# Performance work log

Measured on AMD Instinct MI355X. Metric: run time of the kernel, lower is better.

Reference implementation:

```python
import jax, jax.numpy as jnp
import numpy as np

KERNEL_SIZE = 5


def setup_inputs() -> dict:
    key = jax.random.key(0)
    k1, k2 = jax.random.split(key)
    x = jax.random.normal(k1, (4, 32, 256, 256), dtype=jnp.float32)
    kernel = jax.random.normal(k2, (4, KERNEL_SIZE * KERNEL_SIZE, 256, 256), dtype=jnp.float32)
    return {"x": x, "kernel": kernel}


def reference(x, kernel):
    k = KERNEL_SIZE
    b, kk, h, w = kernel.shape
    # softmax over the k*k dim (original permutes to channels-last then softmax dim=-1)
    kern = jax.nn.softmax(jnp.transpose(kernel, (0, 2, 3, 1)), axis=-1)  # [b,h,w,k*k]
    pad = (k - 1) // 2
    # replicate padding on spatial dims
    xp = jnp.pad(x, ((0, 0), (0, 0), (pad, pad), (pad, pad)), mode="edge")
    # unfold: patch index order is di*k + dj (height offset first), matching torch unfold(2).unfold(3)
    patches = jnp.stack(
        [xp[:, :, i:i + h, j:j + w] for i in range(k) for j in range(k)], axis=-1
    )  # [b,c,h,w,k*k]
    # per-pixel softmax-weighted local sum; kernel broadcast over channel dim
    out = jnp.sum(patches * kern[:, None, :, :, :], axis=-1)  # [b,c,h,w]
    return out
```

## Files before the change

kernel.cpp:

```cpp
#include <hip/hip_runtime.h>

#define HW    256
#define HW2   (HW*HW)
#define KTAPS 25
#define TW    32
#define TH    8
#define LW    36
#define LH    12
#define NEL   (LW*LH)
#define NSTG  7
#define CPB   8
#define C     32

__device__ __forceinline__ void stage_issue(float r[NSTG], const float* __restrict__ xc,
                                            int lane, int h0, int w0) {
#pragma unroll
    for (int k = 0; k < NSTG; ++k) {
        int idx = lane + k * 64;
        if (idx < NEL) {
            int i  = idx / LW;
            int j  = idx - i * LW;
            int hh = min(max(h0 + i - 2, 0), HW - 1);
            int ww = min(max(w0 + j - 2, 0), HW - 1);
            r[k] = xc[hh * HW + ww];
        }
    }
}

__global__ __launch_bounds__(64, 3) void ddown_kernel(
    const float* __restrict__ x,
    const float* __restrict__ kern,
    float* __restrict__ out)
{
    __shared__ __align__(16) float xt[NEL];

    const int lane = threadIdx.x;
    const int txq  = lane & 7;
    const int ty   = lane >> 3;
    const int w0   = blockIdx.x * TW;
    const int h0   = blockIdx.y * TH;
    const int b    = blockIdx.z >> 2;
    const int c0   = (blockIdx.z & 3) * CPB;

    const int h = h0 + ty;
    const int w = w0 + txq * 4;

    const float* xb = x + (size_t)(b * C + c0) * HW2;

    float r[NSTG];
    stage_issue(r, xb, lane, h0, w0);

    const float* kb = kern + (size_t)b * KTAPS * HW2 + h * HW + w;
    float4 wt[KTAPS];
    float sx = 0.f, sy = 0.f, sz = 0.f, sw = 0.f;
#pragma unroll
    for (int j = 0; j < KTAPS; ++j) {
        float4 v = *(const float4*)(kb + (size_t)j * HW2);
        v.x = __expf(v.x); v.y = __expf(v.y); v.z = __expf(v.z); v.w = __expf(v.w);
        sx += v.x; sy += v.y; sz += v.z; sw += v.w;
        wt[j] = v;
    }
    const float ix = 1.f / sx, iy = 1.f / sy, iz = 1.f / sz, iw = 1.f / sw;

    float* ob = out + (size_t)(b * C + c0) * HW2 + h * HW + w;

    for (int cc = 0; cc < CPB; ++cc) {
#pragma unroll
        for (int k = 0; k < NSTG; ++k) {
            int idx = lane + k * 64;
            if (idx < NEL) xt[idx] = r[k];
        }
        if (cc + 1 < CPB) stage_issue(r, xb + (size_t)(cc + 1) * HW2, lane, h0, w0);

        float ax = 0.f, ay = 0.f, az = 0.f, aw = 0.f;
#pragma unroll
        for (int di = 0; di < 5; ++di) {
            const float* row = &xt[(ty + di) * LW + txq * 4];
            float4 pa = *(const float4*)(row);
            float4 pb = *(const float4*)(row + 4);
            float w8[8] = {pa.x, pa.y, pa.z, pa.w, pb.x, pb.y, pb.z, pb.w};
#pragma unroll
            for (int dj = 0; dj < 5; ++dj) {
                float4 wv = wt[di * 5 + dj];
                ax += wv.x * w8[dj + 0];
                ay += wv.y * w8[dj + 1];
                az += wv.z * w8[dj + 2];
                aw += wv.w * w8[dj + 3];
            }
        }
        float4 res = { ax * ix, ay * iy, az * iz, aw * iw };
        *(float4*)(ob + (size_t)cc * HW2) = res;
    }
}

extern "C" void kernel_launch(void* const* d_in, const int* in_sizes, int n_in,
                              void* d_out, int out_size, void* d_ws, size_t ws_size,
                              hipStream_t stream) {
    const float* x    = (const float*)d_in[0];
    const float* kern = (const float*)d_in[1];
    float* out        = (float*)d_out;

    dim3 grid(HW / TW, HW / TH, 4 * 4);
    ddown_kernel<<<grid, 64, 0, stream>>>(x, kern, out);
}
```

Baseline: 109.8 us.

## Replace LDS-tiled kernel with one-thread-per-pixel row kernel looping all channels

```diff
diff --git a/kernel.cpp b/kernel.cpp
--- a/kernel.cpp
+++ b/kernel.cpp
@@ -1,95 +1,72 @@
 #include <hip/hip_runtime.h>
 
-#define HW    256
-#define HW2   (HW*HW)
-#define KTAPS 25
-#define TW    32
-#define TH    8
-#define LW    36
-#define LH    12
-#define NEL   (LW*LH)
-#define NSTG  7
-#define CPB   8
-#define C     32
+#define HW   256
+#define HW2  (HW*HW)
+#define KT   25
+#define C    32
 
-__device__ __forceinline__ void stage_issue(float r[NSTG], const float* __restrict__ xc,
-                                            int lane, int h0, int w0) {
-#pragma unroll
-    for (int k = 0; k < NSTG; ++k) {
-        int idx = lane + k * 64;
-        if (idx < NEL) {
-            int i  = idx / LW;
-            int j  = idx - i * LW;
-            int hh = min(max(h0 + i - 2, 0), HW - 1);
-            int ww = min(max(w0 + j - 2, 0), HW - 1);
-            r[k] = xc[hh * HW + ww];
-        }
-    }
-}
+typedef float f4a4 __attribute__((ext_vector_type(4), aligned(4)));
 
-__global__ __launch_bounds__(64, 3) void ddown_kernel(
+__global__ __launch_bounds__(256, 4) void ddown_kernel(
     const float* __restrict__ x,
     const float* __restrict__ kern,
     float* __restrict__ out)
 {
-    __shared__ __align__(16) float xt[NEL];
+    const int w = threadIdx.x;
+    const int h = blockIdx.x & (HW - 1);
+    const int b = blockIdx.x >> 8;
 
-    const int lane = threadIdx.x;
-    const int txq  = lane & 7;
-    const int ty   = lane >> 3;
-    const int w0   = blockIdx.x * TW;
-    const int h0   = blockIdx.y * TH;
-    const int b    = blockIdx.z >> 2;
-    const int c0   = (blockIdx.z & 3) * CPB;
+    const bool mB = (w == 0), mC = (w == 1), mD = (w == HW - 1);
+    const int  wb = min(max(w - 2, 0), HW - 4);
+    const int  ws = min(w + 2, HW - 1);
 
-    const int h = h0 + ty;
-    const int w = w0 + txq * 4;
+    int hb[5];
+#pragma unroll
+    for (int di = 0; di < 5; ++di)
+        hb[di] = min(max(h + di - 2, 0), HW - 1) * HW;
 
-    const float* xb = x + (size_t)(b * C + c0) * HW2;
-
-    float r[NSTG];
-    stage_issue(r, xb, lane, h0, w0);
-
-    const float* kb = kern + (size_t)b * KTAPS * HW2 + h * HW + w;
-    float4 wt[KTAPS];
-    float sx = 0.f, sy = 0.f, sz = 0.f, sw = 0.f;
+    const float* kb = kern + (size_t)b * KT * HW2 + h * HW + w;
+    float wt[KT];
+    float ssum = 0.f;
 #pragma unroll
-    for (int j = 0; j < KTAPS; ++j) {
-        float4 v = *(const float4*)(kb + (size_t)j * HW2);
-        v.x = __expf(v.x); v.y = __expf(v.y); v.z = __expf(v.z); v.w = __expf(v.w);
-        sx += v.x; sy += v.y; sz += v.z; sw += v.w;
+    for (int j = 0; j < KT; ++j) {
+        float v = __expf(kb[(size_t)j * HW2]);
+        ssum += v;
         wt[j] = v;
     }
-    const float ix = 1.f / sx, iy = 1.f / sy, iz = 1.f / sz, iw = 1.f / sw;
+    const float inv = 1.f / ssum;
+#pragma unroll
+    for (int j = 0; j < KT; ++j) wt[j] *= inv;
 
-    float* ob = out + (size_t)(b * C + c0) * HW2 + h * HW + w;
+#pragma unroll
+    for (int di = 0; di < 5; ++di) {
+        float w0 = wt[di*5+0], w1 = wt[di*5+1], w2 = wt[di*5+2],
+              w3 = wt[di*5+3], w4 = wt[di*5+4];
+        float n0 = mD ? 0.f            : (mB ? (w0 + w1 + w2) : (mC ? (w0 + w1) : w0));
+        float n1 = mD ? w0             : (mB ? w3 : (mC ? w2 : w1));
+        float n2 = mD ? w1             : (mB ? w4 : (mC ? w3 : w2));
+        float n3 = mD ? (w2 + w3 + w4) : (mB ? 0.f : (mC ? w4 : w3));
+        float n4 = (mB || mC || mD) ? 0.f : w4;
+        wt[di*5+0] = n0; wt[di*5+1] = n1; wt[di*5+2] = n2;
+        wt[di*5+3] = n3; wt[di*5+4] = n4;
+    }
 
-    for (int cc = 0; cc < CPB; ++cc) {
+    const float* xb = x   + (size_t)b * C * HW2;
+    float*       ob = out + (size_t)b * C * HW2 + h * HW + w;
+
 #pragma unroll
-        for (int k = 0; k < NSTG; ++k) {
-            int idx = lane + k * 64;
-            if (idx < NEL) xt[idx] = r[k];
-        }
-        if (cc + 1 < CPB) stage_issue(r, xb + (size_t)(cc + 1) * HW2, lane, h0, w0);
-
-        float ax = 0.f, ay = 0.f, az = 0.f, aw = 0.f;
+    for (int c = 0; c < C; ++c) {
+        const float* xc = xb + (size_t)c * HW2;
+        float acc = 0.f;
 #pragma unroll
         for (int di = 0; di < 5; ++di) {
-            const float* row = &xt[(ty + di) * LW + txq * 4];
-            float4 pa = *(const float4*)(row);
-            float4 pb = *(const float4*)(row + 4);
-            float w8[8] = {pa.x, pa.y, pa.z, pa.w, pb.x, pb.y, pb.z, pb.w};
-#pragma unroll
-            for (int dj = 0; dj < 5; ++dj) {
-                float4 wv = wt[di * 5 + dj];
-                ax += wv.x * w8[dj + 0];
-                ay += wv.y * w8[dj + 1];
-                az += wv.z * w8[dj + 2];
-                aw += wv.w * w8[dj + 3];
-            }
+            const float* r = xc + hb[di];
+            f4a4  q  = *(const f4a4*)(r + wb);
+            float sv = r[ws];
+            acc += wt[di*5+0] * q.x + wt[di*5+1] * q.y + wt[di*5+2] * q.z
+                 + wt[di*5+3] * q.w + wt[di*5+4] * sv;
         }
-        float4 res = { ax * ix, ay * iy, az * iz, aw * iw };
-        *(float4*)(ob + (size_t)cc * HW2) = res;
+        ob[(size_t)c * HW2] = acc;
     }
 }
 
@@ -100,6 +77,6 @@
     const float* kern = (const float*)d_in[1];
     float* out        = (float*)d_out;
 
-    dim3 grid(HW / TW, HW / TH, 4 * 4);
-    ddown_kernel<<<grid, 64, 0, stream>>>(x, kern, out);
+    dim3 grid(4 * HW);
+    ddown_kernel<<<grid, 256, 0, stream>>>(x, kern, out);
 }
```

Measured after the change: 120.3 us. 9.6% more time.
